# Performance work log

Measured on AMD Instinct MI355X. Metric: run time of the kernel, lower is better.

## Reference

```python
import jax, jax.numpy as jnp
import numpy as np

V = 50257   # vocab / ouput_size
H = 1024    # hidden_size
L = 4096    # encoder length
NL = 2      # num_layers


def setup_inputs() -> dict:
    key = jax.random.key(0)
    ks = jax.random.split(key, 20)
    s = 0.02
    f32 = jnp.float32
    return {
        "input": jax.random.randint(ks[0], (1, 1), 0, V),
        "hidden_state": jax.random.normal(ks[1], (NL, 1, H), f32),
        "enc_outputs": jax.random.normal(ks[2], (L, H), f32),
        # parameters
        "emb": jax.random.normal(ks[3], (V, H), f32) * s,
        "Wq": jax.random.normal(ks[4], (H, H), f32) * s,
        "Wk": jax.random.normal(ks[5], (H, H), f32) * s,
        "wv": jax.random.normal(ks[6], (H, 1), f32) * s,
        "W_ih0": jax.random.normal(ks[7], (3 * H, 2 * H), f32) * s,
        "W_hh0": jax.random.normal(ks[8], (3 * H, H), f32) * s,
        "b_ih0": jnp.zeros((3 * H,), f32),
        "b_hh0": jnp.zeros((3 * H,), f32),
        "W_ih1": jax.random.normal(ks[9], (3 * H, H), f32) * s,
        "W_hh1": jax.random.normal(ks[10], (3 * H, H), f32) * s,
        "b_ih1": jnp.zeros((3 * H,), f32),
        "b_hh1": jnp.zeros((3 * H,), f32),
        "Wd": jax.random.normal(ks[11], (H, V), f32) * s,
        "bd": jnp.zeros((V,), f32),
    }


def _gru_step(x, h, W_ih, W_hh, b_ih, b_hh):
    # PyTorch GRU cell: gates ordered (reset, update, new)
    gi = W_ih @ x + b_ih          # [3H]
    gh = W_hh @ h + b_hh          # [3H]
    i_r, i_z, i_n = jnp.split(gi, 3)
    h_r, h_z, h_n = jnp.split(gh, 3)
    r = jax.nn.sigmoid(i_r + h_r)
    z = jax.nn.sigmoid(i_z + h_z)
    n = jnp.tanh(i_n + r * h_n)
    return (1.0 - z) * n + z * h


def reference(input, hidden_state, enc_outputs, emb, Wq, Wk, wv,
              W_ih0, W_hh0, b_ih0, b_hh0, W_ih1, W_hh1, b_ih1, b_hh1,
              Wd, bd):
    # embedding + (dropout p=0 is identity) + relu  -> [H]
    emb_vec = jax.nn.relu(emb[input[0, 0]])
    # additive attention: query = last-layer hidden [H], keys/values = enc [L,H]
    query = hidden_state[-1, 0]
    feat = jnp.tanh(query @ Wq + enc_outputs @ Wk)   # [L,H] (broadcast add)
    scores = feat @ wv                               # [L,1]
    attn = jax.nn.softmax(scores, axis=0)            # softmax over L
    context = jnp.sum(attn * enc_outputs, axis=0)    # [H]
    # single-step 2-layer GRU on concat(context, embedded) -> [2H]
    x = jnp.concatenate([context, emb_vec])
    h0n = _gru_step(x, hidden_state[0, 0], W_ih0, W_hh0, b_ih0, b_hh0)
    h1n = _gru_step(h0n, hidden_state[1, 0], W_ih1, W_hh1, b_ih1, b_hh1)
    # dense + log_softmax over vocab
    logits = h1n @ Wd + bd                           # [V]
    logp = jax.nn.log_softmax(logits)[None, :]       # [1,V]
    new_hidden = jnp.stack([h0n, h1n])[:, None, :]   # [NL,1,H]
    return logp, new_hidden
```

## Files before the change

kernel.cpp:

```cpp
#include <hip/hip_runtime.h>
#include <hip/hip_bf16.h>

#define H  1024
#define L  4096
#define V  50257

#define OFF_QW     0
#define OFF_SCORES 1024
#define OFF_X      5120
#define OFF_GI0    7168
#define OFF_GH0    10240
#define OFF_GI1    13312
#define OFF_GH1    16384
#define OFF_LOGITS 19456
#define ZERO_FLOATS (OFF_LOGITS + V)
#define OFF_WKT_BYTES 278880

typedef __bf16 bf8   __attribute__((ext_vector_type(8)));
typedef float  f32x16 __attribute__((ext_vector_type(16)));

__device__ inline unsigned int pack_bf16x2(float lo, float hi) {
    unsigned int ulo = __builtin_bit_cast(unsigned int, lo);
    unsigned int uhi = __builtin_bit_cast(unsigned int, hi);
    return ((uhi + 0x8000u) & 0xFFFF0000u) | ((ulo + 0x8000u) >> 16);
}
__device__ inline unsigned short cvt_bf16(float f) {
    unsigned int u = __builtin_bit_cast(unsigned int, f);
    return (unsigned short)((u + 0x8000u) >> 16);
}

__global__ __launch_bounds__(256) void k_prep(const int* __restrict__ tok,
                                              const float* __restrict__ emb,
                                              const float* __restrict__ hid,
                                              const float* __restrict__ Wq,
                                              const float* __restrict__ Wk,
                                              float* __restrict__ ws,
                                              unsigned short* __restrict__ wkT) {
    __shared__ float tile[32][33];
    const int b = blockIdx.x, t = threadIdx.x;
    if (b < 4) {
        int j = b * 256 + t;
        float v = emb[(size_t)tok[0] * H + j];
        ws[OFF_X + H + j] = fmaxf(v, 0.f);
    } else if (b < 68) {
        int bb = b - 4;
        int j = (bb & 3) * 256 + t;
        int i0 = (bb >> 2) * 64;
        const float* q = hid + H;
        float acc = 0.f;
#pragma unroll 8
        for (int i = i0; i < i0 + 64; ++i) acc += q[i] * Wq[i * H + j];
        atomicAdd(&ws[OFF_QW + j], acc);
    } else {
        int tt = b - 68;
        int tk = tt & 31, tn = tt >> 5;
        int c = t & 31, r0 = t >> 5;
#pragma unroll
        for (int rr = 0; rr < 4; ++rr) {
            int r = r0 + rr * 8;
            tile[r][c] = Wk[(size_t)(tk * 32 + r) * H + tn * 32 + c];
        }
        __syncthreads();
#pragma unroll
        for (int rr = 0; rr < 4; ++rr) {
            int rn = r0 + rr * 8;
            wkT[(size_t)(tn * 32 + rn) * H + tk * 32 + c] = cvt_bf16(tile[c][rn]);
        }
    }
}

__global__ __launch_bounds__(256) void k_gemm_scores(const float* __restrict__ enc,
                                                     const unsigned short* __restrict__ wkT,
                                                     const float* __restrict__ wv,
                                                     float* __restrict__ ws) {
    __shared__ unsigned short As[64][40];
    __shared__ unsigned short Bs[128][40];
    const int t = threadIdx.x, lane = t & 63, w = t >> 6;
    const int m0 = blockIdx.x * 64, n0 = blockIdx.y * 128;

    f32x16 acc0 = {}, acc1 = {};

    const int ar = t >> 2, akq = (t & 3) * 8;
    const int bn = t >> 1, bkh = (t & 1) * 16;

    const int r0 = (w & 1) * 32, c0 = (w >> 1) * 64;
    const int mrow = r0 + (lane & 31);
    const int nrow0 = c0 + (lane & 31), nrow1 = nrow0 + 32;

    for (int k0 = 0; k0 < H; k0 += 32) {
        float4 fa = *(const float4*)(enc + (size_t)(m0 + ar) * H + k0 + akq);
        float4 fb = *(const float4*)(enc + (size_t)(m0 + ar) * H + k0 + akq + 4);
        uint4 wb0 = *(const uint4*)(wkT + (size_t)(n0 + bn) * H + k0 + bkh);
        uint4 wb1 = *(const uint4*)(wkT + (size_t)(n0 + bn) * H + k0 + bkh + 8);
        __syncthreads();
        uint4 pa;
        pa.x = pack_bf16x2(fa.x, fa.y); pa.y = pack_bf16x2(fa.z, fa.w);
        pa.z = pack_bf16x2(fb.x, fb.y); pa.w = pack_bf16x2(fb.z, fb.w);
        *(uint4*)&As[ar][akq] = pa;
        *(uint4*)&Bs[bn][bkh] = wb0;
        *(uint4*)&Bs[bn][bkh + 8] = wb1;
        __syncthreads();
#pragma unroll
        for (int kk = 0; kk < 2; ++kk) {
            int kb = kk * 16 + (lane >> 5) * 8;
            bf8 a  = *(const bf8*)&As[mrow][kb];
            bf8 b0 = *(const bf8*)&Bs[nrow0][kb];
            bf8 b1 = *(const bf8*)&Bs[nrow1][kb];
            acc0 = __builtin_amdgcn_mfma_f32_32x32x16_bf16(a, b0, acc0, 0, 0, 0);
            acc1 = __builtin_amdgcn_mfma_f32_32x32x16_bf16(a, b1, acc1, 0, 0, 0);
        }
    }

    const int n_a = n0 + nrow0, n_b = n0 + nrow1;
    float qwa = ws[OFF_QW + n_a], qwb = ws[OFF_QW + n_b];
    float wva = wv[n_a], wvb = wv[n_b];
    const int rbase = m0 + r0 + 4 * (lane >> 5);
#pragma unroll
    for (int reg = 0; reg < 16; ++reg) {
        float s = tanhf(acc0[reg] + qwa) * wva + tanhf(acc1[reg] + qwb) * wvb;
#pragma unroll
        for (int msk = 1; msk < 32; msk <<= 1) s += __shfl_xor(s, msk);
        if ((lane & 31) == 0) {
            int l = rbase + (reg & 3) + 8 * (reg >> 2);
            atomicAdd(&ws[OFF_SCORES + l], s);
        }
    }
}

__global__ __launch_bounds__(256) void k_context(const float* __restrict__ enc,
                                                 float* __restrict__ ws) {
    __shared__ float red[4];
    const int t = threadIdx.x;
    const float* sc = ws + OFF_SCORES;

    float m = -1e30f;
#pragma unroll
    for (int i = 0; i < 16; ++i) m = fmaxf(m, sc[t + i * 256]);
#pragma unroll
    for (int msk = 1; msk < 64; msk <<= 1) m = fmaxf(m, __shfl_xor(m, msk));
    if ((t & 63) == 0) red[t >> 6] = m;
    __syncthreads();
    m = fmaxf(fmaxf(red[0], red[1]), fmaxf(red[2], red[3]));
    __syncthreads();

    float s = 0.f;
#pragma unroll
    for (int i = 0; i < 16; ++i) s += expf(sc[t + i * 256] - m);
#pragma unroll
    for (int msk = 1; msk < 64; msk <<= 1) s += __shfl_xor(s, msk);
    if ((t & 63) == 0) red[t >> 6] = s;
    __syncthreads();
    float inv = 1.f / (red[0] + red[1] + red[2] + red[3]);

    const int h = blockIdx.x * 256 + t;
    const int l0 = blockIdx.y * 128;
    float acc = 0.f;
#pragma unroll 4
    for (int l = l0; l < l0 + 128; ++l)
        acc += expf(sc[l] - m) * enc[(size_t)l * H + h];
    atomicAdd(&ws[OFF_X + h], acc * inv);
}

__global__ __launch_bounds__(256) void k_gates(const float* __restrict__ Wih,
                                               const float* __restrict__ Whh,
                                               const float* __restrict__ bih,
                                               const float* __restrict__ bhh,
                                               const float* __restrict__ x, int Cx,
                                               const float* __restrict__ h,
                                               float* __restrict__ gi,
                                               float* __restrict__ gh) {
    int b = blockIdx.x;
    bool isH = (b >= 768);
    int row  = (isH ? b - 768 : b) * 4 + (threadIdx.x >> 6);
    int lane = threadIdx.x & 63;
    const float* W    = isH ? Whh : Wih;
    const float* v    = isH ? h : x;
    const float* bias = isH ? bhh : bih;
    int C       = isH ? H : Cx;
    float* out  = isH ? gh : gi;

    const float4* Wr = (const float4*)(W + (size_t)row * C);
    const float4* v4 = (const float4*)v;
    float acc = 0.f;
    int n4 = C >> 2;
    for (int c = lane; c < n4; c += 64) {
        float4 wv4 = Wr[c], xx = v4[c];
        acc += wv4.x * xx.x + wv4.y * xx.y + wv4.z * xx.z + wv4.w * xx.w;
    }
#pragma unroll
    for (int off = 32; off; off >>= 1) acc += __shfl_down(acc, off);
    if (lane == 0) out[row] = acc + bias[row];
}

__global__ __launch_bounds__(256) void k_gates1(const float* __restrict__ Wih,
                                                const float* __restrict__ Whh,
                                                const float* __restrict__ bih,
                                                const float* __restrict__ bhh,
                                                const float* __restrict__ gi0,
                                                const float* __restrict__ gh0,
                                                const float* __restrict__ hid,
                                                float* __restrict__ h0n_out,
                                                float* __restrict__ gi,
                                                float* __restrict__ gh) {
    const int b = blockIdx.x, t = threadIdx.x;
    const int lane = t & 63;
    if (b < 768) {
        __shared__ float xs[H];
#pragma unroll
        for (int jj = 0; jj < 4; ++jj) {
            int j = t + jj * 256;
            float r = 1.f / (1.f + expf(-(gi0[j] + gh0[j])));
            float z = 1.f / (1.f + expf(-(gi0[H + j] + gh0[H + j])));
            float n = tanhf(gi0[2 * H + j] + r * gh0[2 * H + j]);
            float h0 = (1.f - z) * n + z * hid[j];
            xs[j] = h0;
            if (b == 0) h0n_out[j] = h0;
        }
        __syncthreads();
        int row = b * 4 + (t >> 6);
        const float4* Wr = (const float4*)(Wih + (size_t)row * H);
        float acc = 0.f;
        for (int c = lane; c < H / 4; c += 64) {
            float4 wv4 = Wr[c];
            float4 xx = *(const float4*)&xs[c * 4];
            acc += wv4.x * xx.x + wv4.y * xx.y + wv4.z * xx.z + wv4.w * xx.w;
        }
#pragma unroll
        for (int off = 32; off; off >>= 1) acc += __shfl_down(acc, off);
        if (lane == 0) gi[row] = acc + bih[row];
    } else {
        int row = (b - 768) * 4 + (t >> 6);
        const float4* Wr = (const float4*)(Whh + (size_t)row * H);
        const float4* h4 = (const float4*)(hid + H);
        float acc = 0.f;
        for (int c = lane; c < H / 4; c += 64) {
            float4 wv4 = Wr[c], xx = h4[c];
            acc += wv4.x * xx.x + wv4.y * xx.y + wv4.z * xx.z + wv4.w * xx.w;
        }
#pragma unroll
        for (int off = 32; off; off >>= 1) acc += __shfl_down(acc, off);
        if (lane == 0) gh[row] = acc + bhh[row];
    }
}

__global__ __launch_bounds__(256) void k_logits(const float* __restrict__ Wd,
                                                const float* __restrict__ bd,
                                                const float* __restrict__ gi1,
                                                const float* __restrict__ gh1,
                                                const float* __restrict__ hid,
                                                float* __restrict__ h1n_out,
                                                float* __restrict__ ws) {
    __shared__ float h1s[H];
    const int t = threadIdx.x;
#pragma unroll
    for (int jj = 0; jj < 4; ++jj) {
        int j = t + jj * 256;
        float r = 1.f / (1.f + expf(-(gi1[j] + gh1[j])));
        float z = 1.f / (1.f + expf(-(gi1[H + j] + gh1[H + j])));
        float n = tanhf(gi1[2 * H + j] + r * gh1[2 * H + j]);
        float h1 = (1.f - z) * n + z * hid[H + j];
        h1s[j] = h1;
        if (blockIdx.x == 0 && blockIdx.y == 0) h1n_out[j] = h1;
    }
    __syncthreads();
    int v = blockIdx.x * 256 + t;
    if (v >= V) return;
    int k0 = blockIdx.y * 128;
    float acc = (blockIdx.y == 0) ? bd[v] : 0.f;
    const float* Wp = Wd + (size_t)k0 * V + v;
#pragma unroll 8
    for (int k = 0; k < 128; ++k) acc += h1s[k0 + k] * Wp[(size_t)k * V];
    atomicAdd(&ws[OFF_LOGITS + v], acc);
}

__global__ __launch_bounds__(1024) void k_logsoftmax(const float* __restrict__ lg,
                                                     float* __restrict__ out) {
    __shared__ float red[16];
    const int tid = threadIdx.x;

    float m = -1e30f;
    for (int v = tid; v < V; v += 1024) m = fmaxf(m, lg[v]);
#pragma unroll
    for (int off = 32; off; off >>= 1) m = fmaxf(m, __shfl_down(m, off));
    if ((tid & 63) == 0) red[tid >> 6] = m;
    __syncthreads();
    if (tid == 0) {
        float mm = red[0];
        for (int w = 1; w < 16; ++w) mm = fmaxf(mm, red[w]);
        red[0] = mm;
    }
    __syncthreads();
    m = red[0];
    __syncthreads();

    float s = 0.f;
    for (int v = tid; v < V; v += 1024) s += expf(lg[v] - m);
#pragma unroll
    for (int off = 32; off; off >>= 1) s += __shfl_down(s, off);
    if ((tid & 63) == 0) red[tid >> 6] = s;
    __syncthreads();
    if (tid == 0) {
        float tt = 0.f;
        for (int w = 0; w < 16; ++w) tt += red[w];
        red[0] = tt;
    }
    __syncthreads();
    float lse = m + logf(red[0]);

    for (int v = tid; v < V; v += 1024) out[v] = lg[v] - lse;
}

extern "C" void kernel_launch(void* const* d_in, const int* in_sizes, int n_in,
                              void* d_out, int out_size, void* d_ws, size_t ws_size,
                              hipStream_t stream) {
    const int*   tok  = (const int*)d_in[0];
    const float* hid  = (const float*)d_in[1];
    const float* enc  = (const float*)d_in[2];
    const float* emb  = (const float*)d_in[3];
    const float* Wq   = (const float*)d_in[4];
    const float* Wk   = (const float*)d_in[5];
    const float* wv   = (const float*)d_in[6];
    const float* Wih0 = (const float*)d_in[7];
    const float* Whh0 = (const float*)d_in[8];
    const float* bih0 = (const float*)d_in[9];
    const float* bhh0 = (const float*)d_in[10];
    const float* Wih1 = (const float*)d_in[11];
    const float* Whh1 = (const float*)d_in[12];
    const float* bih1 = (const float*)d_in[13];
    const float* bhh1 = (const float*)d_in[14];
    const float* Wd   = (const float*)d_in[15];
    const float* bd   = (const float*)d_in[16];
    float* out = (float*)d_out;
    float* ws  = (float*)d_ws;
    unsigned short* wkT = (unsigned short*)((char*)d_ws + OFF_WKT_BYTES);

    hipMemsetAsync(ws, 0, ZERO_FLOATS * sizeof(float), stream);

    k_prep<<<1092, 256, 0, stream>>>(tok, emb, hid, Wq, Wk, ws, wkT);
    k_gemm_scores<<<dim3(L / 64, H / 128), 256, 0, stream>>>(enc, wkT, wv, ws);
    k_context<<<dim3(4, 32), 256, 0, stream>>>(enc, ws);
    k_gates<<<1536, 256, 0, stream>>>(Wih0, Whh0, bih0, bhh0,
                                      ws + OFF_X, 2 * H, hid,
                                      ws + OFF_GI0, ws + OFF_GH0);
    k_gates1<<<1536, 256, 0, stream>>>(Wih1, Whh1, bih1, bhh1,
                                       ws + OFF_GI0, ws + OFF_GH0, hid,
                                       out + V, ws + OFF_GI1, ws + OFF_GH1);
    k_logits<<<dim3((V + 255) / 256, 8), 256, 0, stream>>>(Wd, bd,
                                       ws + OFF_GI1, ws + OFF_GH1, hid,
                                       out + V + H, ws);
    k_logsoftmax<<<1, 1024, 0, stream>>>(ws + OFF_LOGITS, out);
}
```

Before: 533.2 us.

## Fuse whole decoder step into one cooperative persistent kernel with grid syncs

Replaces the memset plus seven separate kernel launches with a single cooperative kernel of 512 blocks that runs each stage in a grid-stride loop and separates stages with grid-wide syncs. The hidden-to-hidden gate GEMVs for both layers are moved into the first phase so they overlap with prep work. The GRU elementwise step is recomputed redundantly per block, and log-softmax is spread across all blocks using partial max and sum buffers. This removes launch gaps and the single-block log-softmax tail, at the cost of grid-barrier overhead and of falling back to the old multi-kernel path if the cooperative launch fails.

```diff
diff --git a/kernel.cpp b/kernel.cpp
--- a/kernel.cpp
+++ b/kernel.cpp
@@ -1,9 +1,15 @@
 #include <hip/hip_runtime.h>
+#include <hip/hip_cooperative_groups.h>
 #include <hip/hip_bf16.h>
+
+namespace cg = cooperative_groups;
 
 #define H  1024
 #define L  4096
 #define V  50257
+
+#define NB 512
+#define NT 256
 
 #define OFF_QW     0
 #define OFF_SCORES 1024
@@ -13,8 +19,10 @@
 #define OFF_GI1    13312
 #define OFF_GH1    16384
 #define OFF_LOGITS 19456
+#define OFF_PMAX   (OFF_LOGITS + V)
+#define OFF_PSUM   (OFF_PMAX + NB)
 #define ZERO_FLOATS (OFF_LOGITS + V)
-#define OFF_WKT_BYTES 278880
+#define OFF_WKT_BYTES 283008
 
 typedef __bf16 bf8   __attribute__((ext_vector_type(8)));
 typedef float  f32x16 __attribute__((ext_vector_type(16)));
@@ -27,6 +35,293 @@
 __device__ inline unsigned short cvt_bf16(float f) {
     unsigned int u = __builtin_bit_cast(unsigned int, f);
     return (unsigned short)((u + 0x8000u) >> 16);
+}
+
+struct Prm {
+    const int*   tok;
+    const float* hid;
+    const float* enc;
+    const float* emb;
+    const float* Wq;
+    const float* Wk;
+    const float* wv;
+    const float* Wih0;
+    const float* Whh0;
+    const float* bih0;
+    const float* bhh0;
+    const float* Wih1;
+    const float* Whh1;
+    const float* bih1;
+    const float* bhh1;
+    const float* Wd;
+    const float* bd;
+    float* out;
+    float* ws;
+    unsigned short* wkT;
+};
+
+__global__ __launch_bounds__(NT, 2) void k_all(Prm p) {
+    cg::grid_group gg = cg::this_grid();
+    const int bid = blockIdx.x, t = threadIdx.x;
+    float* __restrict__ ws = p.ws;
+
+    __shared__ float tile[32][33];
+    __shared__ unsigned short As[64][40];
+    __shared__ unsigned short Bs[128][40];
+    __shared__ float xs[H];
+    __shared__ float red[16];
+
+    {
+        int g = bid * NT + t;
+        if (g < 4096) ws[OFF_SCORES + g] = 0.f;
+        if (g < 1024) ws[OFF_X + g] = 0.f;
+        if (g < V)    ws[OFF_LOGITS + g] = 0.f;
+    }
+    for (int vb = bid; vb < 2568; vb += NB) {
+        if (vb < 4) {
+            int j = vb * 256 + t;
+            float v = p.emb[(size_t)p.tok[0] * H + j];
+            ws[OFF_X + H + j] = fmaxf(v, 0.f);
+        } else if (vb < 8) {
+            int j = (vb - 4) * 256 + t;
+            const float* q = p.hid + H;
+            float acc = 0.f;
+#pragma unroll 8
+            for (int i = 0; i < H; ++i) acc += q[i] * p.Wq[(size_t)i * H + j];
+            ws[OFF_QW + j] = acc;
+        } else if (vb < 1032) {
+            int tt = vb - 8, tk = tt & 31, tn = tt >> 5;
+            int c = t & 31, r0 = t >> 5;
+#pragma unroll
+            for (int rr = 0; rr < 4; ++rr) {
+                int r = r0 + rr * 8;
+                tile[r][c] = p.Wk[(size_t)(tk * 32 + r) * H + tn * 32 + c];
+            }
+            __syncthreads();
+#pragma unroll
+            for (int rr = 0; rr < 4; ++rr) {
+                int rn = r0 + rr * 8;
+                p.wkT[(size_t)(tn * 32 + rn) * H + tk * 32 + c] = cvt_bf16(tile[c][rn]);
+            }
+            __syncthreads();
+        } else {
+            bool l1 = (vb >= 1800);
+            int row  = (vb - (l1 ? 1800 : 1032)) * 4 + (t >> 6);
+            int lane = t & 63;
+            const float*  W  = l1 ? p.Whh1 : p.Whh0;
+            const float*  b  = l1 ? p.bhh1 : p.bhh0;
+            const float4* hv = (const float4*)(l1 ? p.hid + H : p.hid);
+            const float4* Wr = (const float4*)(W + (size_t)row * H);
+            float acc = 0.f;
+#pragma unroll
+            for (int c = lane; c < H / 4; c += 64) {
+                float4 w = Wr[c], x = hv[c];
+                acc += w.x * x.x + w.y * x.y + w.z * x.z + w.w * x.w;
+            }
+#pragma unroll
+            for (int off = 32; off; off >>= 1) acc += __shfl_down(acc, off);
+            if (lane == 0) ws[(l1 ? OFF_GH1 : OFF_GH0) + row] = acc + b[row];
+        }
+    }
+    gg.sync();
+
+    for (int vb = bid; vb < 512; vb += NB) {
+        const int lane = t & 63, w = t >> 6;
+        const int m0 = (vb & 63) * 64, n0 = (vb >> 6) * 128;
+        f32x16 acc0 = {}, acc1 = {};
+        const int ar = t >> 2, akq = (t & 3) * 8;
+        const int bn = t >> 1, bkh = (t & 1) * 16;
+        const int r0 = (w & 1) * 32, c0 = (w >> 1) * 64;
+        const int mrow = r0 + (lane & 31);
+        const int nrow0 = c0 + (lane & 31), nrow1 = nrow0 + 32;
+
+        for (int k0 = 0; k0 < H; k0 += 32) {
+            float4 fa = *(const float4*)(p.enc + (size_t)(m0 + ar) * H + k0 + akq);
+            float4 fb = *(const float4*)(p.enc + (size_t)(m0 + ar) * H + k0 + akq + 4);
+            uint4 wb0 = *(const uint4*)(p.wkT + (size_t)(n0 + bn) * H + k0 + bkh);
+            uint4 wb1 = *(const uint4*)(p.wkT + (size_t)(n0 + bn) * H + k0 + bkh + 8);
+            __syncthreads();
+            uint4 pa;
+            pa.x = pack_bf16x2(fa.x, fa.y); pa.y = pack_bf16x2(fa.z, fa.w);
+            pa.z = pack_bf16x2(fb.x, fb.y); pa.w = pack_bf16x2(fb.z, fb.w);
+            *(uint4*)&As[ar][akq] = pa;
+            *(uint4*)&Bs[bn][bkh] = wb0;
+            *(uint4*)&Bs[bn][bkh + 8] = wb1;
+            __syncthreads();
+#pragma unroll
+            for (int kk = 0; kk < 2; ++kk) {
+                int kb = kk * 16 + (lane >> 5) * 8;
+                bf8 a  = *(const bf8*)&As[mrow][kb];
+                bf8 b0 = *(const bf8*)&Bs[nrow0][kb];
+                bf8 b1 = *(const bf8*)&Bs[nrow1][kb];
+                acc0 = __builtin_amdgcn_mfma_f32_32x32x16_bf16(a, b0, acc0, 0, 0, 0);
+                acc1 = __builtin_amdgcn_mfma_f32_32x32x16_bf16(a, b1, acc1, 0, 0, 0);
+            }
+        }
+        const int n_a = n0 + nrow0, n_b = n0 + nrow1;
+        float qwa = ws[OFF_QW + n_a], qwb = ws[OFF_QW + n_b];
+        float wva = p.wv[n_a], wvb = p.wv[n_b];
+        const int rbase = m0 + r0 + 4 * (lane >> 5);
+#pragma unroll
+        for (int reg = 0; reg < 16; ++reg) {
+            float s = tanhf(acc0[reg] + qwa) * wva + tanhf(acc1[reg] + qwb) * wvb;
+#pragma unroll
+            for (int msk = 1; msk < 32; msk <<= 1) s += __shfl_xor(s, msk);
+            if ((lane & 31) == 0)
+                atomicAdd(&ws[OFF_SCORES + rbase + (reg & 3) + 8 * (reg >> 2)], s);
+        }
+    }
+    gg.sync();
+
+    for (int vb = bid; vb < 512; vb += NB) {
+        const float* sc = ws + OFF_SCORES;
+        float m = -1e30f;
+#pragma unroll
+        for (int i = 0; i < 16; ++i) m = fmaxf(m, sc[t + i * 256]);
+#pragma unroll
+        for (int msk = 1; msk < 64; msk <<= 1) m = fmaxf(m, __shfl_xor(m, msk));
+        if ((t & 63) == 0) red[t >> 6] = m;
+        __syncthreads();
+        m = fmaxf(fmaxf(red[0], red[1]), fmaxf(red[2], red[3]));
+        __syncthreads();
+        float s = 0.f;
+#pragma unroll
+        for (int i = 0; i < 16; ++i) s += expf(sc[t + i * 256] - m);
+#pragma unroll
+        for (int msk = 1; msk < 64; msk <<= 1) s += __shfl_xor(s, msk);
+        if ((t & 63) == 0) red[t >> 6] = s;
+        __syncthreads();
+        float inv = 1.f / (red[0] + red[1] + red[2] + red[3]);
+
+        const int h = (vb & 3) * 256 + t;
+        const int l0 = (vb >> 2) * 32;
+        float acc = 0.f;
+#pragma unroll 4
+        for (int l = l0; l < l0 + 32; ++l)
+            acc += expf(sc[l] - m) * p.enc[(size_t)l * H + h];
+        atomicAdd(&ws[OFF_X + h], acc * inv);
+        __syncthreads();
+    }
+    gg.sync();
+
+    for (int vb = bid; vb < 768; vb += NB) {
+        int row = vb * 4 + (t >> 6), lane = t & 63;
+        const float4* Wr = (const float4*)(p.Wih0 + (size_t)row * (2 * H));
+        const float4* x4 = (const float4*)(ws + OFF_X);
+        float acc = 0.f;
+#pragma unroll
+        for (int c = lane; c < 2 * H / 4; c += 64) {
+            float4 w = Wr[c], x = x4[c];
+            acc += w.x * x.x + w.y * x.y + w.z * x.z + w.w * x.w;
+        }
+#pragma unroll
+        for (int off = 32; off; off >>= 1) acc += __shfl_down(acc, off);
+        if (lane == 0) ws[OFF_GI0 + row] = acc + p.bih0[row];
+    }
+    gg.sync();
+
+    {
+#pragma unroll
+        for (int jj = 0; jj < 4; ++jj) {
+            int j = t + jj * 256;
+            float r = 1.f / (1.f + expf(-(ws[OFF_GI0 + j] + ws[OFF_GH0 + j])));
+            float z = 1.f / (1.f + expf(-(ws[OFF_GI0 + H + j] + ws[OFF_GH0 + H + j])));
+            float n = tanhf(ws[OFF_GI0 + 2 * H + j] + r * ws[OFF_GH0 + 2 * H + j]);
+            float h0 = (1.f - z) * n + z * p.hid[j];
+            xs[j] = h0;
+            if (bid == 0) p.out[V + j] = h0;
+        }
+        __syncthreads();
+        for (int vb = bid; vb < 768; vb += NB) {
+            int row = vb * 4 + (t >> 6), lane = t & 63;
+            const float4* Wr = (const float4*)(p.Wih1 + (size_t)row * H);
+            float acc = 0.f;
+#pragma unroll
+            for (int c = lane; c < H / 4; c += 64) {
+                float4 w = Wr[c];
+                float4 x = *(const float4*)&xs[c * 4];
+                acc += w.x * x.x + w.y * x.y + w.z * x.z + w.w * x.w;
+            }
+#pragma unroll
+            for (int off = 32; off; off >>= 1) acc += __shfl_down(acc, off);
+            if (lane == 0) ws[OFF_GI1 + row] = acc + p.bih1[row];
+        }
+    }
+    gg.sync();
+
+    {
+#pragma unroll
+        for (int jj = 0; jj < 4; ++jj) {
+            int j = t + jj * 256;
+            float r = 1.f / (1.f + expf(-(ws[OFF_GI1 + j] + ws[OFF_GH1 + j])));
+            float z = 1.f / (1.f + expf(-(ws[OFF_GI1 + H + j] + ws[OFF_GH1 + H + j])));
+            float n = tanhf(ws[OFF_GI1 + 2 * H + j] + r * ws[OFF_GH1 + 2 * H + j]);
+            float h1 = (1.f - z) * n + z * p.hid[H + j];
+            xs[j] = h1;
+            if (bid == 0) p.out[V + H + j] = h1;
+        }
+        __syncthreads();
+        const int NV5 = (V + 511) / 512;
+        for (int vb = bid; vb < NV5 * 8; vb += NB) {
+            int v0 = (vb >> 3) * 512, k0 = (vb & 7) * 128;
+            int va = v0 + t, vb2 = v0 + 256 + t;
+            int vac = va  < V ? va  : V - 1;
+            int vbc = vb2 < V ? vb2 : V - 1;
+            float acca = 0.f, accb = 0.f;
+            const float* Wp = p.Wd + (size_t)k0 * V;
+#pragma unroll 8
+            for (int k = 0; k < 128; ++k) {
+                float xk = xs[k0 + k];
+                const float* row = Wp + (size_t)k * V;
+                acca += xk * row[vac];
+                accb += xk * row[vbc];
+            }
+            if (va  < V) atomicAdd(&ws[OFF_LOGITS + va],  acca + (k0 == 0 ? p.bd[va]  : 0.f));
+            if (vb2 < V) atomicAdd(&ws[OFF_LOGITS + vb2], accb + (k0 == 0 ? p.bd[vb2] : 0.f));
+        }
+    }
+    gg.sync();
+
+    float gmax;
+    {
+        int g = bid * NT + t;
+        float m = (g < V) ? ws[OFF_LOGITS + g] : -1e30f;
+#pragma unroll
+        for (int msk = 1; msk < 64; msk <<= 1) m = fmaxf(m, __shfl_xor(m, msk));
+        if ((t & 63) == 0) red[t >> 6] = m;
+        __syncthreads();
+        if (t == 0) ws[OFF_PMAX + bid] = fmaxf(fmaxf(red[0], red[1]), fmaxf(red[2], red[3]));
+    }
+    gg.sync();
+    {
+        float m = -1e30f;
+        for (int i = t; i < NB; i += NT) m = fmaxf(m, ws[OFF_PMAX + i]);
+#pragma unroll
+        for (int msk = 1; msk < 64; msk <<= 1) m = fmaxf(m, __shfl_xor(m, msk));
+        if ((t & 63) == 0) red[t >> 6] = m;
+        __syncthreads();
+        gmax = fmaxf(fmaxf(red[0], red[1]), fmaxf(red[2], red[3]));
+        __syncthreads();
+        int g = bid * NT + t;
+        float s = (g < V) ? expf(ws[OFF_LOGITS + g] - gmax) : 0.f;
+#pragma unroll
+        for (int msk = 1; msk < 64; msk <<= 1) s += __shfl_xor(s, msk);
+        if ((t & 63) == 0) red[t >> 6] = s;
+        __syncthreads();
+        if (t == 0) ws[OFF_PSUM + bid] = red[0] + red[1] + red[2] + red[3];
+    }
+    gg.sync();
+    {
+        float s = 0.f;
+        for (int i = t; i < NB; i += NT) s += ws[OFF_PSUM + i];
+#pragma unroll
+        for (int msk = 1; msk < 64; msk <<= 1) s += __shfl_xor(s, msk);
+        if ((t & 63) == 0) red[t >> 6] = s;
+        __syncthreads();
+        float lse = gmax + logf(red[0] + red[1] + red[2] + red[3]);
+        int g = bid * NT + t;
+        if (g < V) p.out[g] = ws[OFF_LOGITS + g] - lse;
+    }
 }
 
 __global__ __launch_bounds__(256) void k_prep(const int* __restrict__ tok,
@@ -77,16 +372,12 @@
     __shared__ unsigned short Bs[128][40];
     const int t = threadIdx.x, lane = t & 63, w = t >> 6;
     const int m0 = blockIdx.x * 64, n0 = blockIdx.y * 128;
-
     f32x16 acc0 = {}, acc1 = {};
-
     const int ar = t >> 2, akq = (t & 3) * 8;
     const int bn = t >> 1, bkh = (t & 1) * 16;
-
     const int r0 = (w & 1) * 32, c0 = (w >> 1) * 64;
     const int mrow = r0 + (lane & 31);
     const int nrow0 = c0 + (lane & 31), nrow1 = nrow0 + 32;
-
     for (int k0 = 0; k0 < H; k0 += 32) {
         float4 fa = *(const float4*)(enc + (size_t)(m0 + ar) * H + k0 + akq);
         float4 fb = *(const float4*)(enc + (size_t)(m0 + ar) * H + k0 + akq + 4);
@@ -110,7 +401,6 @@
             acc1 = __builtin_amdgcn_mfma_f32_32x32x16_bf16(a, b1, acc1, 0, 0, 0);
         }
     }
-
     const int n_a = n0 + nrow0, n_b = n0 + nrow1;
     float qwa = ws[OFF_QW + n_a], qwb = ws[OFF_QW + n_b];
     float wva = wv[n_a], wvb = wv[n_b];
@@ -132,7 +422,6 @@
     __shared__ float red[4];
     const int t = threadIdx.x;
     const float* sc = ws + OFF_SCORES;
-
     float m = -1e30f;
 #pragma unroll
     for (int i = 0; i < 16; ++i) m = fmaxf(m, sc[t + i * 256]);
@@ -142,7 +431,6 @@
     __syncthreads();
     m = fmaxf(fmaxf(red[0], red[1]), fmaxf(red[2], red[3]));
     __syncthreads();
-
     float s = 0.f;
 #pragma unroll
     for (int i = 0; i < 16; ++i) s += expf(sc[t + i * 256] - m);
@@ -151,7 +439,6 @@
     if ((t & 63) == 0) red[t >> 6] = s;
     __syncthreads();
     float inv = 1.f / (red[0] + red[1] + red[2] + red[3]);
-
     const int h = blockIdx.x * 256 + t;
     const int l0 = blockIdx.y * 128;
     float acc = 0.f;
@@ -178,7 +465,6 @@
     const float* bias = isH ? bhh : bih;
     int C       = isH ? H : Cx;
     float* out  = isH ? gh : gi;
-
     const float4* Wr = (const float4*)(W + (size_t)row * C);
     const float4* v4 = (const float4*)v;
     float acc = 0.f;
@@ -277,7 +563,6 @@
                                                      float* __restrict__ out) {
     __shared__ float red[16];
     const int tid = threadIdx.x;
-
     float m = -1e30f;
     for (int v = tid; v < V; v += 1024) m = fmaxf(m, lg[v]);
 #pragma unroll
@@ -292,7 +577,6 @@
     __syncthreads();
     m = red[0];
     __syncthreads();
-
     float s = 0.f;
     for (int v = tid; v < V; v += 1024) s += expf(lg[v] - m);
 #pragma unroll
@@ -306,7 +590,6 @@
     }
     __syncthreads();
     float lse = m + logf(red[0]);
-
     for (int v = tid; v < V; v += 1024) out[v] = lg[v] - lse;
 }
 
@@ -334,19 +617,27 @@
     float* ws  = (float*)d_ws;
     unsigned short* wkT = (unsigned short*)((char*)d_ws + OFF_WKT_BYTES);
 
-    hipMemsetAsync(ws, 0, ZERO_FLOATS * sizeof(float), stream);
-
-    k_prep<<<1092, 256, 0, stream>>>(tok, emb, hid, Wq, Wk, ws, wkT);
-    k_gemm_scores<<<dim3(L / 64, H / 128), 256, 0, stream>>>(enc, wkT, wv, ws);
-    k_context<<<dim3(4, 32), 256, 0, stream>>>(enc, ws);
-    k_gates<<<1536, 256, 0, stream>>>(Wih0, Whh0, bih0, bhh0,
-                                      ws + OFF_X, 2 * H, hid,
-                                      ws + OFF_GI0, ws + OFF_GH0);
-    k_gates1<<<1536, 256, 0, stream>>>(Wih1, Whh1, bih1, bhh1,
-                                       ws + OFF_GI0, ws + OFF_GH0, hid,
-                                       out + V, ws + OFF_GI1, ws + OFF_GH1);
-    k_logits<<<dim3((V + 255) / 256, 8), 256, 0, stream>>>(Wd, bd,
-                                       ws + OFF_GI1, ws + OFF_GH1, hid,
-                                       out + V + H, ws);
-    k_logsoftmax<<<1, 1024, 0, stream>>>(ws + OFF_LOGITS, out);
-}
+    Prm prm{tok, hid, enc, emb, Wq, Wk, wv,
+            Wih0, Whh0, bih0, bhh0, Wih1, Whh1, bih1, bhh1,
+            Wd, bd, out, ws, wkT};
+    void* args[] = {(void*)&prm};
+    hipError_t e = hipLaunchCooperativeKernel((const void*)k_all,
+                                              dim3(NB), dim3(NT), args, 0, stream);
+    if (e != hipSuccess) {
+        (void)hipGetLastError();
+        hipMemsetAsync(ws, 0, ZERO_FLOATS * sizeof(float), stream);
+        k_prep<<<1092, 256, 0, stream>>>(tok, emb, hid, Wq, Wk, ws, wkT);
+        k_gemm_scores<<<dim3(L / 64, H / 128), 256, 0, stream>>>(enc, wkT, wv, ws);
+        k_context<<<dim3(4, 32), 256, 0, stream>>>(enc, ws);
+        k_gates<<<1536, 256, 0, stream>>>(Wih0, Whh0, bih0, bhh0,
+                                          ws + OFF_X, 2 * H, hid,
+                                          ws + OFF_GI0, ws + OFF_GH0);
+        k_gates1<<<1536, 256, 0, stream>>>(Wih1, Whh1, bih1, bhh1,
+                                           ws + OFF_GI0, ws + OFF_GH0, hid,
+                                           out + V, ws + OFF_GI1, ws + OFF_GH1);
+        k_logits<<<dim3((V + 255) / 256, 8), 256, 0, stream>>>(Wd, bd,
+                                           ws + OFF_GI1, ws + OFF_GH1, hid,
+                                           out + V + H, ws);
+        k_logsoftmax<<<1, 1024, 0, stream>>>(ws + OFF_LOGITS, out);
+    }
+}
```

Measured after the change: 1.022 ms. 1.92x slower.

## Hoist hidden GEMVs into prep, parallelize log-softmax, widen logits tiles

Applied to the files above, without the earlier changes.

Moves the W_hh·h GEMVs for both GRU layers into the prep kernel, since they depend only on inputs, which takes them off the serial critical path. Replaces the single-block log-softmax with a two-pass, multi-block partial max/sum reduction. The logits kernel now has each thread compute two vocab columns, and the attention weights are precomputed into shared memory inside k_context. Together these cut serial work and launch-dependent latency, at the cost of a larger prep grid and one extra kernel launch.

```diff
diff --git a/kernel.cpp b/kernel.cpp
--- a/kernel.cpp
+++ b/kernel.cpp
@@ -13,8 +13,10 @@
 #define OFF_GI1    13312
 #define OFF_GH1    16384
 #define OFF_LOGITS 19456
+#define OFF_PMAX   (OFF_LOGITS + V)
+#define OFF_PSUM   (OFF_PMAX + 256)
 #define ZERO_FLOATS (OFF_LOGITS + V)
-#define OFF_WKT_BYTES 278880
+#define OFF_WKT_BYTES 283008
 
 typedef __bf16 bf8   __attribute__((ext_vector_type(8)));
 typedef float  f32x16 __attribute__((ext_vector_type(16)));
@@ -34,6 +36,10 @@
                                               const float* __restrict__ hid,
                                               const float* __restrict__ Wq,
                                               const float* __restrict__ Wk,
+                                              const float* __restrict__ Whh0,
+                                              const float* __restrict__ bhh0,
+                                              const float* __restrict__ Whh1,
+                                              const float* __restrict__ bhh1,
                                               float* __restrict__ ws,
                                               unsigned short* __restrict__ wkT) {
     __shared__ float tile[32][33];
@@ -51,7 +57,7 @@
 #pragma unroll 8
         for (int i = i0; i < i0 + 64; ++i) acc += q[i] * Wq[i * H + j];
         atomicAdd(&ws[OFF_QW + j], acc);
-    } else {
+    } else if (b < 1092) {
         int tt = b - 68;
         int tk = tt & 31, tn = tt >> 5;
         int c = t & 31, r0 = t >> 5;
@@ -66,6 +72,23 @@
             int rn = r0 + rr * 8;
             wkT[(size_t)(tn * 32 + rn) * H + tk * 32 + c] = cvt_bf16(tile[c][rn]);
         }
+    } else {
+        bool l1 = (b >= 1860);
+        int row  = (b - (l1 ? 1860 : 1092)) * 4 + (t >> 6);
+        int lane = t & 63;
+        const float*  W  = l1 ? Whh1 : Whh0;
+        const float*  bi = l1 ? bhh1 : bhh0;
+        const float4* hv = (const float4*)(l1 ? hid + H : hid);
+        const float4* Wr = (const float4*)(W + (size_t)row * H);
+        float acc = 0.f;
+#pragma unroll
+        for (int c = lane; c < H / 4; c += 64) {
+            float4 w = Wr[c], x = hv[c];
+            acc += w.x * x.x + w.y * x.y + w.z * x.z + w.w * x.w;
+        }
+#pragma unroll
+        for (int off = 32; off; off >>= 1) acc += __shfl_down(acc, off);
+        if (lane == 0) ws[(l1 ? OFF_GH1 : OFF_GH0) + row] = acc + bi[row];
     }
 }
 
@@ -130,6 +153,7 @@
 __global__ __launch_bounds__(256) void k_context(const float* __restrict__ enc,
                                                  float* __restrict__ ws) {
     __shared__ float red[4];
+    __shared__ float ps[128];
     const int t = threadIdx.x;
     const float* sc = ws + OFF_SCORES;
 
@@ -152,95 +176,69 @@
     __syncthreads();
     float inv = 1.f / (red[0] + red[1] + red[2] + red[3]);
 
+    const int l0 = blockIdx.y * 128;
+    if (t < 128) ps[t] = expf(sc[l0 + t] - m) * inv;
+    __syncthreads();
+
     const int h = blockIdx.x * 256 + t;
-    const int l0 = blockIdx.y * 128;
     float acc = 0.f;
 #pragma unroll 4
-    for (int l = l0; l < l0 + 128; ++l)
-        acc += expf(sc[l] - m) * enc[(size_t)l * H + h];
-    atomicAdd(&ws[OFF_X + h], acc * inv);
-}
-
-__global__ __launch_bounds__(256) void k_gates(const float* __restrict__ Wih,
-                                               const float* __restrict__ Whh,
-                                               const float* __restrict__ bih,
-                                               const float* __restrict__ bhh,
-                                               const float* __restrict__ x, int Cx,
-                                               const float* __restrict__ h,
-                                               float* __restrict__ gi,
-                                               float* __restrict__ gh) {
-    int b = blockIdx.x;
-    bool isH = (b >= 768);
-    int row  = (isH ? b - 768 : b) * 4 + (threadIdx.x >> 6);
+    for (int l = 0; l < 128; ++l)
+        acc += ps[l] * enc[(size_t)(l0 + l) * H + h];
+    atomicAdd(&ws[OFF_X + h], acc);
+}
+
+__global__ __launch_bounds__(256) void k_gi0(const float* __restrict__ Wih,
+                                             const float* __restrict__ bih,
+                                             const float* __restrict__ ws_x,
+                                             float* __restrict__ gi) {
+    int row = blockIdx.x * 4 + (threadIdx.x >> 6);
     int lane = threadIdx.x & 63;
-    const float* W    = isH ? Whh : Wih;
-    const float* v    = isH ? h : x;
-    const float* bias = isH ? bhh : bih;
-    int C       = isH ? H : Cx;
-    float* out  = isH ? gh : gi;
-
-    const float4* Wr = (const float4*)(W + (size_t)row * C);
-    const float4* v4 = (const float4*)v;
+    const float4* Wr = (const float4*)(Wih + (size_t)row * (2 * H));
+    const float4* v4 = (const float4*)ws_x;
     float acc = 0.f;
-    int n4 = C >> 2;
-    for (int c = lane; c < n4; c += 64) {
-        float4 wv4 = Wr[c], xx = v4[c];
-        acc += wv4.x * xx.x + wv4.y * xx.y + wv4.z * xx.z + wv4.w * xx.w;
+#pragma unroll
+    for (int c = lane; c < 2 * H / 4; c += 64) {
+        float4 w = Wr[c], xx = v4[c];
+        acc += w.x * xx.x + w.y * xx.y + w.z * xx.z + w.w * xx.w;
     }
 #pragma unroll
     for (int off = 32; off; off >>= 1) acc += __shfl_down(acc, off);
-    if (lane == 0) out[row] = acc + bias[row];
-}
-
-__global__ __launch_bounds__(256) void k_gates1(const float* __restrict__ Wih,
-                                                const float* __restrict__ Whh,
-                                                const float* __restrict__ bih,
-                                                const float* __restrict__ bhh,
-                                                const float* __restrict__ gi0,
-                                                const float* __restrict__ gh0,
-                                                const float* __restrict__ hid,
-                                                float* __restrict__ h0n_out,
-                                                float* __restrict__ gi,
-                                                float* __restrict__ gh) {
-    const int b = blockIdx.x, t = threadIdx.x;
-    const int lane = t & 63;
-    if (b < 768) {
-        __shared__ float xs[H];
-#pragma unroll
-        for (int jj = 0; jj < 4; ++jj) {
-            int j = t + jj * 256;
-            float r = 1.f / (1.f + expf(-(gi0[j] + gh0[j])));
-            float z = 1.f / (1.f + expf(-(gi0[H + j] + gh0[H + j])));
-            float n = tanhf(gi0[2 * H + j] + r * gh0[2 * H + j]);
-            float h0 = (1.f - z) * n + z * hid[j];
-            xs[j] = h0;
-            if (b == 0) h0n_out[j] = h0;
-        }
-        __syncthreads();
-        int row = b * 4 + (t >> 6);
-        const float4* Wr = (const float4*)(Wih + (size_t)row * H);
-        float acc = 0.f;
-        for (int c = lane; c < H / 4; c += 64) {
-            float4 wv4 = Wr[c];
-            float4 xx = *(const float4*)&xs[c * 4];
-            acc += wv4.x * xx.x + wv4.y * xx.y + wv4.z * xx.z + wv4.w * xx.w;
-        }
-#pragma unroll
-        for (int off = 32; off; off >>= 1) acc += __shfl_down(acc, off);
-        if (lane == 0) gi[row] = acc + bih[row];
-    } else {
-        int row = (b - 768) * 4 + (t >> 6);
-        const float4* Wr = (const float4*)(Whh + (size_t)row * H);
-        const float4* h4 = (const float4*)(hid + H);
-        float acc = 0.f;
-        for (int c = lane; c < H / 4; c += 64) {
-            float4 wv4 = Wr[c], xx = h4[c];
-            acc += wv4.x * xx.x + wv4.y * xx.y + wv4.z * xx.z + wv4.w * xx.w;
-        }
-#pragma unroll
-        for (int off = 32; off; off >>= 1) acc += __shfl_down(acc, off);
-        if (lane == 0) gh[row] = acc + bhh[row];
-    }
+    if (lane == 0) gi[row] = acc + bih[row];
+}
+
+__global__ __launch_bounds__(256) void k_gi1(const float* __restrict__ Wih,
+                                             const float* __restrict__ bih,
+                                             const float* __restrict__ gi0,
+                                             const float* __restrict__ gh0,
+                                             const float* __restrict__ hid,
+                                             float* __restrict__ h0n_out,
+                                             float* __restrict__ gi) {
+    __shared__ float xs[H];
+    const int b = blockIdx.x, t = threadIdx.x, lane = t & 63;
+#pragma unroll
+    for (int jj = 0; jj < 4; ++jj) {
+        int j = t + jj * 256;
+        float r = 1.f / (1.f + expf(-(gi0[j] + gh0[j])));
+        float z = 1.f / (1.f + expf(-(gi0[H + j] + gh0[H + j])));
+        float n = tanhf(gi0[2 * H + j] + r * gh0[2 * H + j]);
+        float h0 = (1.f - z) * n + z * hid[j];
+        xs[j] = h0;
+        if (b == 0) h0n_out[j] = h0;
+    }
+    __syncthreads();
+    int row = b * 4 + (t >> 6);
+    const float4* Wr = (const float4*)(Wih + (size_t)row * H);
+    float acc = 0.f;
+#pragma unroll
+    for (int c = lane; c < H / 4; c += 64) {
+        float4 w = Wr[c];
+        float4 xx = *(const float4*)&xs[c * 4];
+        acc += w.x * xx.x + w.y * xx.y + w.z * xx.z + w.w * xx.w;
+    }
+#pragma unroll
+    for (int off = 32; off; off >>= 1) acc += __shfl_down(acc, off);
+    if (lane == 0) gi[row] = acc + bih[row];
 }
 
 __global__ __launch_bounds__(256) void k_logits(const float* __restrict__ Wd,
@@ -263,51 +261,73 @@
         if (blockIdx.x == 0 && blockIdx.y == 0) h1n_out[j] = h1;
     }
     __syncthreads();
-    int v = blockIdx.x * 256 + t;
-    if (v >= V) return;
-    int k0 = blockIdx.y * 128;
-    float acc = (blockIdx.y == 0) ? bd[v] : 0.f;
-    const float* Wp = Wd + (size_t)k0 * V + v;
+    const int v0 = blockIdx.x * 512, k0 = blockIdx.y * 128;
+    const int va = v0 + t, vb = v0 + 256 + t;
+    const int vac = va < V ? va : V - 1;
+    const int vbc = vb < V ? vb : V - 1;
+    float acca = 0.f, accb = 0.f;
+    const float* Wp = Wd + (size_t)k0 * V;
 #pragma unroll 8
-    for (int k = 0; k < 128; ++k) acc += h1s[k0 + k] * Wp[(size_t)k * V];
-    atomicAdd(&ws[OFF_LOGITS + v], acc);
-}
-
-__global__ __launch_bounds__(1024) void k_logsoftmax(const float* __restrict__ lg,
-                                                     float* __restrict__ out) {
-    __shared__ float red[16];
-    const int tid = threadIdx.x;
-
-    float m = -1e30f;
-    for (int v = tid; v < V; v += 1024) m = fmaxf(m, lg[v]);
-#pragma unroll
-    for (int off = 32; off; off >>= 1) m = fmaxf(m, __shfl_down(m, off));
-    if ((tid & 63) == 0) red[tid >> 6] = m;
-    __syncthreads();
-    if (tid == 0) {
-        float mm = red[0];
-        for (int w = 1; w < 16; ++w) mm = fmaxf(mm, red[w]);
-        red[0] = mm;
-    }
-    __syncthreads();
-    m = red[0];
-    __syncthreads();
-
-    float s = 0.f;
-    for (int v = tid; v < V; v += 1024) s += expf(lg[v] - m);
-#pragma unroll
-    for (int off = 32; off; off >>= 1) s += __shfl_down(s, off);
-    if ((tid & 63) == 0) red[tid >> 6] = s;
-    __syncthreads();
-    if (tid == 0) {
-        float tt = 0.f;
-        for (int w = 0; w < 16; ++w) tt += red[w];
-        red[0] = tt;
-    }
-    __syncthreads();
-    float lse = m + logf(red[0]);
-
-    for (int v = tid; v < V; v += 1024) out[v] = lg[v] - lse;
+    for (int k = 0; k < 128; ++k) {
+        float xk = h1s[k0 + k];
+        const float* row = Wp + (size_t)k * V;
+        acca += xk * row[vac];
+        accb += xk * row[vbc];
+    }
+    if (va < V) atomicAdd(&ws[OFF_LOGITS + va], acca + (k0 == 0 ? bd[va] : 0.f));
+    if (vb < V) atomicAdd(&ws[OFF_LOGITS + vb], accb + (k0 == 0 ? bd[vb] : 0.f));
+}
+
+__global__ __launch_bounds__(256) void k_lsm1(const float* __restrict__ lg,
+                                              float* __restrict__ ws) {
+    __shared__ float red[4];
+    const int b = blockIdx.x, t = threadIdx.x;
+    const int g = b * 256 + t;
+    float x = (g < V) ? lg[g] : -1e30f;
+
+    float m = x;
+#pragma unroll
+    for (int msk = 1; msk < 64; msk <<= 1) m = fmaxf(m, __shfl_xor(m, msk));
+    if ((t & 63) == 0) red[t >> 6] = m;
+    __syncthreads();
+    m = fmaxf(fmaxf(red[0], red[1]), fmaxf(red[2], red[3]));
+    __syncthreads();
+
+    float s = (g < V) ? expf(x - m) : 0.f;
+#pragma unroll
+    for (int msk = 1; msk < 64; msk <<= 1) s += __shfl_xor(s, msk);
+    if ((t & 63) == 0) red[t >> 6] = s;
+    __syncthreads();
+    if (t == 0) {
+        ws[OFF_PMAX + b] = m;
+        ws[OFF_PSUM + b] = red[0] + red[1] + red[2] + red[3];
+    }
+}
+
+__global__ __launch_bounds__(256) void k_lsm2(const float* __restrict__ lg,
+                                              const float* __restrict__ ws,
+                                              float* __restrict__ out) {
+    __shared__ float red[4];
+    const int b = blockIdx.x, t = threadIdx.x;
+
+    float pm = (t < 197) ? ws[OFF_PMAX + t] : -1e30f;
+    float m = pm;
+#pragma unroll
+    for (int msk = 1; msk < 64; msk <<= 1) m = fmaxf(m, __shfl_xor(m, msk));
+    if ((t & 63) == 0) red[t >> 6] = m;
+    __syncthreads();
+    m = fmaxf(fmaxf(red[0], red[1]), fmaxf(red[2], red[3]));
+    __syncthreads();
+
+    float s = (t < 197) ? ws[OFF_PSUM + t] * expf(pm - m) : 0.f;
+#pragma unroll
+    for (int msk = 1; msk < 64; msk <<= 1) s += __shfl_xor(s, msk);
+    if ((t & 63) == 0) red[t >> 6] = s;
+    __syncthreads();
+    float lse = m + logf(red[0] + red[1] + red[2] + red[3]);
+
+    const int g = b * 256 + t;
+    if (g < V) out[g] = lg[g] - lse;
 }
 
 extern "C" void kernel_launch(void* const* d_in, const int* in_sizes, int n_in,
@@ -336,17 +356,15 @@
 
     hipMemsetAsync(ws, 0, ZERO_FLOATS * sizeof(float), stream);
 
-    k_prep<<<1092, 256, 0, stream>>>(tok, emb, hid, Wq, Wk, ws, wkT);
+    k_prep<<<2628, 256, 0, stream>>>(tok, emb, hid, Wq, Wk,
+                                     Whh0, bhh0, Whh1, bhh1, ws, wkT);
     k_gemm_scores<<<dim3(L / 64, H / 128), 256, 0, stream>>>(enc, wkT, wv, ws);
     k_context<<<dim3(4, 32), 256, 0, stream>>>(enc, ws);
-    k_gates<<<1536, 256, 0, stream>>>(Wih0, Whh0, bih0, bhh0,
-                                      ws + OFF_X, 2 * H, hid,
-                                      ws + OFF_GI0, ws + OFF_GH0);
-    k_gates1<<<1536, 256, 0, stream>>>(Wih1, Whh1, bih1, bhh1,
-                                       ws + OFF_GI0, ws + OFF_GH0, hid,
-                                       out + V, ws + OFF_GI1, ws + OFF_GH1);
-    k_logits<<<dim3((V + 255) / 256, 8), 256, 0, stream>>>(Wd, bd,
-                                       ws + OFF_GI1, ws + OFF_GH1, hid,
-                                       out + V + H, ws);
-    k_logsoftmax<<<1, 1024, 0, stream>>>(ws + OFF_LOGITS, out);
-}
+    k_gi0<<<768, 256, 0, stream>>>(Wih0, bih0, ws + OFF_X, ws + OFF_GI0);
+    k_gi1<<<768, 256, 0, stream>>>(Wih1, bih1, ws + OFF_GI0, ws + OFF_GH0,
+                                   hid, out + V, ws + OFF_GI1);
+    k_logits<<<dim3(99, 8), 256, 0, stream>>>(Wd, bd, ws + OFF_GI1, ws + OFF_GH1,
+                                              hid, out + V + H, ws);
+    k_lsm1<<<197, 256, 0, stream>>>(ws + OFF_LOGITS, ws);
+    k_lsm2<<<197, 256, 0, stream>>>(ws + OFF_LOGITS, ws, out);
+}
```

After: 518.2 us. 1.03x faster.
